# Performance work log

Measured on AMD Instinct MI355X. Metric: run time of the kernel, lower is better.

The kernel has to match this reference:

```python
import jax, jax.numpy as jnp
import numpy as np

KS = 7
HEADS = 8


def _conv1x1(a, w, b):
    # a: (B,Cin,H,W), w: (Cout,Cin), b: (Cout,)
    return jnp.einsum('bchw,oc->bohw', a, w) + b[None, :, None, None]


def _unfold2d(a, ks):
    # a: (B,C,Hp,Wp) -> (B,C,H,W,ks,ks) sliding windows, stride 1
    H = a.shape[2] - ks + 1
    W = a.shape[3] - ks + 1
    ii = jnp.arange(H)[:, None] + jnp.arange(ks)[None, :]  # (H,ks)
    jj = jnp.arange(W)[:, None] + jnp.arange(ks)[None, :]  # (W,ks)
    return a[:, :, ii[:, None, :, None], jj[None, :, None, :]]


def setup_inputs() -> dict:
    key = jax.random.key(0)
    ks = jax.random.split(key, 10)
    B, C, H, W = 4, 128, 56, 56
    x = jax.random.normal(ks[0], (B, C, H, W), dtype=jnp.float32)
    sc = 1.0 / np.sqrt(C)
    q_w = jax.random.normal(ks[1], (C, C), dtype=jnp.float32) * sc
    q_b = jax.random.normal(ks[2], (C,), dtype=jnp.float32) * 0.01
    k_w = jax.random.normal(ks[3], (C, C), dtype=jnp.float32) * sc
    k_b = jax.random.normal(ks[4], (C,), dtype=jnp.float32) * 0.01
    v_w = jax.random.normal(ks[5], (C, C), dtype=jnp.float32) * sc
    v_b = jax.random.normal(ks[6], (C,), dtype=jnp.float32) * 0.01
    rel_h = jax.random.normal(ks[7], (C // 2, KS, 1), dtype=jnp.float32)
    rel_w = jax.random.normal(ks[8], (C // 2, 1, KS), dtype=jnp.float32)
    return {'x': x, 'q_w': q_w, 'q_b': q_b, 'k_w': k_w, 'k_b': k_b,
            'v_w': v_w, 'v_b': v_b, 'rel_h': rel_h, 'rel_w': rel_w}


def reference(x, q_w, q_b, k_w, k_b, v_w, v_b, rel_h, rel_w):
    B, C, H, W = x.shape
    dkh = C // HEADS
    K2 = KS * KS
    pl = (KS - 1) // 2
    pr = KS - 1 - pl
    xp = jnp.pad(x, ((0, 0), (0, 0), (pl, pr), (pl, pr)))

    k = _conv1x1(xp, k_w, k_b)
    v = _conv1x1(xp, v_w, v_b)
    q = _conv1x1(x, q_w, q_b)

    # unfold K/V into (B,C,H,W,KS,KS) then reshape exactly as torch does
    # (this reshape intermixes channel/window axes; replicated faithfully)
    k6 = _unfold2d(k, KS).reshape(B, HEADS, H, W, dkh, K2)
    v6 = _unfold2d(v, KS).reshape(B, HEADS, H, W, dkh, K2)
    q6 = q.reshape(B, HEADS, H, W, dkh, 1)

    # q^T k over the dkh axis -> (B,heads,H,W,KS,KS)
    qk = jnp.einsum('bhxyd,bhxydk->bhxyk', q6[..., 0], k6)
    qk = qk.reshape(B, HEADS, H, W, KS, KS)

    # einsum 'bhxydz,cij->bhxyij' has no shared index: factorizes as
    # (sum over d,z of q) * (sum over c of rel)
    qsum = q6.sum(axis=(4, 5))  # (B,heads,H,W)
    qk = qk + qsum[..., None, None] * rel_h.sum(axis=0)  # (KS,1) broadcast
    qk = qk + qsum[..., None, None] * rel_w.sum(axis=0)  # (1,KS) broadcast

    w = jax.nn.softmax(qk.reshape(B, HEADS, H, W, K2), axis=-1)
    out = jnp.einsum('bhxyk,bhxydk->bhxyd', w, v6)  # (B,heads,H,W,dvh)
    return out.reshape(B, C, H, W)
```

## Files before the change

### kernel.cpp

```cpp
#include <hip/hip_runtime.h>
#include <hip/hip_bf16.h>
#include <math.h>

#define NB    4
#define NC    128
#define NPIX  3136
#define CHW   401408
#define KVP   3968
#define SKS   68
#define STS   19

template <int CTRL, int RM>
__device__ __forceinline__ float dpp_mov(float x, float old) {
    return __int_as_float(__builtin_amdgcn_update_dpp(
        __float_as_int(old), __float_as_int(x), CTRL, RM, 0xf, false));
}
__device__ __forceinline__ float wave_max(float x) {
    x = fmaxf(x, dpp_mov<0x111, 0xf>(x, x));
    x = fmaxf(x, dpp_mov<0x112, 0xf>(x, x));
    x = fmaxf(x, dpp_mov<0x114, 0xf>(x, x));
    x = fmaxf(x, dpp_mov<0x118, 0xf>(x, x));
    x = fmaxf(x, dpp_mov<0x142, 0xa>(x, x));
    x = fmaxf(x, dpp_mov<0x143, 0xc>(x, x));
    return __int_as_float(__builtin_amdgcn_readlane(__float_as_int(x), 63));
}
__device__ __forceinline__ float wave_sum(float x) {
    x = x + dpp_mov<0x111, 0xf>(x, 0.f);
    x = x + dpp_mov<0x112, 0xf>(x, 0.f);
    x = x + dpp_mov<0x114, 0xf>(x, 0.f);
    x = x + dpp_mov<0x118, 0xf>(x, 0.f);
    x = x + dpp_mov<0x142, 0xa>(x, 0.f);
    x = x + dpp_mov<0x143, 0xc>(x, 0.f);
    return __int_as_float(__builtin_amdgcn_readlane(__float_as_int(x), 63));
}

__global__ __launch_bounds__(256) void prep_kernel(
    const float* __restrict__ qw, const float* __restrict__ kw,
    const float* __restrict__ vw,
    const float* __restrict__ kb, const float* __restrict__ vb,
    const float* __restrict__ rel_h, const float* __restrict__ rel_w,
    float* __restrict__ kpad, float* __restrict__ vpad,
    float* __restrict__ w4q, float* __restrict__ w4k, float* __restrict__ w4v,
    float* __restrict__ rb)
{
    int idx = blockIdx.x * 256 + threadIdx.x;
    {
        int img = idx / 708;
        int hl = idx - img * 708;
        int p;
        if (hl < 186) {
            int r = hl / 62;
            p = r * 64 + (hl - r * 62);
        } else if (hl < 372) {
            int j = hl - 186;
            int r = j / 62;
            p = (59 + r) * 64 + (j - r * 62);
        } else {
            int j = hl - 372;
            int r = j / 6, cc = j - r * 6;
            p = (r + 3) * 64 + (cc < 3 ? cc : cc + 56);
        }
        int ch = img & 127;
        size_t o = (size_t)img * KVP + p;
        kpad[o] = kb[ch];
        vpad[o] = vb[ch];
    }
    if (idx < 3 * 16384) {
        int m = idx >> 14;
        int r = idx & 16383;
        int cc = r & 3;
        int t = r >> 2;
        int o = t & 127;
        int c4 = t >> 7;
        const float* src = (m == 0) ? qw : (m == 1) ? kw : vw;
        float* dst = (m == 0) ? w4q : (m == 1) ? w4k : w4v;
        dst[r] = src[o * 128 + c4 * 4 + cc];
    }
    if (idx < 14) {
        const float* src = (idx < 7) ? rel_h : rel_w;
        int off = (idx < 7) ? idx : idx - 7;
        float s = 0.f;
        for (int c = 0; c < 64; ++c) s += src[c * 7 + off];
        rb[idx] = s;
    }
}

__global__ __launch_bounds__(256) void conv_kernel(
    const float* __restrict__ x,
    const float* __restrict__ w4q, const float* __restrict__ w4k,
    const float* __restrict__ w4v,
    const float* __restrict__ qb, const float* __restrict__ kb,
    const float* __restrict__ vb,
    float* __restrict__ q, float* __restrict__ kpad, float* __restrict__ vpad)
{
    __shared__ float sx[128 * 16];
    __shared__ float st[3 * 128 * STS];
    int bid = blockIdx.x;
    int tile = bid % 196;
    int b = bid / 196;
    int pix0 = tile * 16;
    const float* xb = x + b * CHW + pix0;

    for (int i = threadIdx.x; i < 512; i += 256) {
        int c = i >> 2, p4 = (i & 3) * 4;
        *(float4*)(sx + c * 16 + p4) = *(const float4*)(xb + c * NPIX + p4);
    }
    __syncthreads();

    int lane = threadIdx.x & 63;
    int wave = threadIdx.x >> 6;
    int o = wave * 32 + (lane & 31);
    int ph = (lane >> 5) * 8;
    const float4* Wq = (const float4*)w4q + o;
    const float4* Wk = (const float4*)w4k + o;
    const float4* Wv = (const float4*)w4v + o;

    float4 wqc = Wq[0], wkc = Wk[0], wvc = Wv[0];
    float aq[8] = {}, ak[8] = {}, av[8] = {};
    #pragma unroll 1
    for (int c4 = 0; c4 < 32; ++c4) {
        float4 xs[8];
        #pragma unroll
        for (int cc = 0; cc < 4; ++cc) {
            xs[2 * cc]     = *(const float4*)(sx + (c4 * 4 + cc) * 16 + ph);
            xs[2 * cc + 1] = *(const float4*)(sx + (c4 * 4 + cc) * 16 + ph + 4);
        }
        float4 wq4 = wqc, wk4 = wkc, wv4 = wvc;
        if (c4 < 31) {
            wqc = Wq[(c4 + 1) * 128];
            wkc = Wk[(c4 + 1) * 128];
            wvc = Wv[(c4 + 1) * 128];
        }
        float wqr[4] = {wq4.x, wq4.y, wq4.z, wq4.w};
        float wkr[4] = {wk4.x, wk4.y, wk4.z, wk4.w};
        float wvr[4] = {wv4.x, wv4.y, wv4.z, wv4.w};
        #pragma unroll
        for (int cc = 0; cc < 4; ++cc) {
            float4 xa = xs[2 * cc], xc = xs[2 * cc + 1];
            float xv[8] = {xa.x, xa.y, xa.z, xa.w, xc.x, xc.y, xc.z, xc.w};
            #pragma unroll
            for (int p = 0; p < 8; ++p) {
                aq[p] += wqr[cc] * xv[p];
                ak[p] += wkr[cc] * xv[p];
                av[p] += wvr[cc] * xv[p];
            }
        }
    }
    float bq = qb[o], bk = kb[o], bv = vb[o];
    float* wrq = st + o * STS + ph;
    float* wrk = st + 128 * STS + o * STS + ph;
    float* wrv = st + 2 * 128 * STS + o * STS + ph;
    #pragma unroll
    for (int p = 0; p < 8; ++p) {
        wrq[p] = aq[p] + bq;
        wrk[p] = ak[p] + bk;
        wrv[p] = av[p] + bv;
    }
    __syncthreads();

    int pix = threadIdx.x & 15;
    int o8 = (threadIdx.x >> 4) * 8;
    int pp = pix0 + pix;
    int yy = pp / 56, xx = pp - yy * 56;
    int po = (yy + 3) * 64 + xx + 3;
    float* qd = q + b * CHW + pix0 + pix;
    float* kd = kpad + (size_t)b * 128 * KVP + po;
    float* vd = vpad + (size_t)b * 128 * KVP + po;
    #pragma unroll
    for (int i = 0; i < 8; ++i) {
        int r = o8 + i;
        qd[r * NPIX] = st[r * STS + pix];
        kd[(size_t)r * KVP] = st[128 * STS + r * STS + pix];
        vd[(size_t)r * KVP] = st[2 * 128 * STS + r * STS + pix];
    }
}

__global__ __launch_bounds__(256) void attn_kernel(
    const float* __restrict__ q, const float* __restrict__ kpad,
    const float* __restrict__ vpad,
    const float* __restrict__ rb, float* __restrict__ out)
{
    __shared__ __align__(16) float sK[20 * SKS];
    __shared__ __align__(16) float sV[21 * SKS];
    __shared__ float sW[4 * 64];
    int bid = blockIdx.x;
    int qpart = bid & 3;
    int bc = bid >> 2;
    const float* qc = q + bc * NPIX + 784 * qpart;
    float* oc = out + bc * NPIX + 784 * qpart;
    int qr0 = 14 * qpart;
    const float* kp0 = kpad + (size_t)bc * KVP + qr0 * 64;
    const float* vp0 = vpad + (size_t)bc * KVP + qr0 * 64;

    for (int i = threadIdx.x; i < 320; i += 256) {
        int yy = i >> 4, c16 = i & 15;
        if (c16 < 15) {
            float4 kv4 = *(const float4*)(kp0 + yy * 64 + c16 * 4);
            float4 vv4 = *(const float4*)(vp0 + yy * 64 + c16 * 4);
            *(float4*)(sK + yy * SKS + c16 * 4) = kv4;
            *(float4*)(sV + yy * SKS + c16 * 4) = vv4;
        } else {
            float2 kv2 = *(const float2*)(kp0 + yy * 64 + 60);
            float2 vv2 = *(const float2*)(vp0 + yy * 64 + 60);
            *(float2*)(sK + yy * SKS + 60) = kv2;
            *(float2*)(sV + yy * SKS + 60) = vv2;
        }
    }
    for (int i = threadIdx.x; i < SKS; i += 256) sV[20 * SKS + i] = 0.f;

    int lane = threadIdx.x & 63;
    int wave = threadIdx.x >> 6;
    int k2 = min(lane, 48);
    int di = k2 / 7, dj = k2 - di * 7;
    float rbias = rb[di] + rb[7 + dj];
    int koff = di * SKS + dj;
    int t16 = lane & 15, p = lane >> 4;
    float* sWw = sW + wave * 64;

    int ul0 = wave * 16;
    int y0 = 0, x0 = ul0;
    float4 p0 = *(const float4*)(qc + ul0);
    float4 p1 = *(const float4*)(qc + ul0 + 4);
    float4 p2 = *(const float4*)(qc + ul0 + 8);
    float4 p3 = *(const float4*)(qc + ul0 + 12);
    __syncthreads();

    for (int gl = wave; gl < 49; gl += 4) {
        float4 q0 = p0, q1 = p1, q2 = p2, q3 = p3;
        if (gl + 4 < 49) {
            int un = ul0 + 64;
            p0 = *(const float4*)(qc + un);
            p1 = *(const float4*)(qc + un + 4);
            p2 = *(const float4*)(qc + un + 8);
            p3 = *(const float4*)(qc + un + 12);
        }
        float qa[16] = {q0.x, q0.y, q0.z, q0.w, q1.x, q1.y, q1.z, q1.w,
                        q2.x, q2.y, q2.z, q2.w, q3.x, q3.y, q3.z, q3.w};
        float qs = 0.f;
        #pragma unroll
        for (int t = 0; t < 16; ++t) qs += qa[t];

        float acc = 0.f;
        const float* kb_ = sK + y0 * SKS + x0 + koff;
        if (x0 != 48) {
            #pragma unroll
            for (int t = 0; t < 16; ++t) acc += qa[t] * kb_[t];
        } else {
            const float* kb2 = sK + (y0 + 1) * SKS + koff;
            #pragma unroll
            for (int t = 0; t < 8; ++t) acc += qa[t] * kb_[t];
            #pragma unroll
            for (int t = 0; t < 8; ++t) acc += qa[8 + t] * kb2[t];
        }
        float val = (lane < 49) ? (acc + qs * rbias) : -1e30f;

        float mS = wave_max(val);
        float e = __expf(val - mS);
        float sS = wave_sum(e);
        float wgt = e * __builtin_amdgcn_rcpf(sS);
        sWw[lane] = wgt;

        int u = ul0 + t16;
        int yt = u / 56;
        int xt = u - yt * 56;
        const float* vbase = sV + yt * SKS + xt + p * (2 * SKS);
        const float* wbase = sWw + p * 14;
        float o0 = 0.f, o1 = 0.f;
        #pragma unroll
        for (int j = 0; j < 7; ++j) o0 += wbase[j] * vbase[j];
        #pragma unroll
        for (int j = 0; j < 7; ++j) o1 += wbase[7 + j] * vbase[SKS + j];
        float oacc = o0 + o1;
        oacc += __shfl_xor(oacc, 16);
        oacc += __shfl_xor(oacc, 32);
        if (lane < 16) oc[ul0 + lane] = oacc;

        ul0 += 64;
        x0 += 8; y0 += 1;
        if (x0 >= 56) { x0 -= 56; ++y0; }
    }
}

extern "C" void kernel_launch(void* const* d_in, const int* in_sizes, int n_in,
                              void* d_out, int out_size, void* d_ws, size_t ws_size,
                              hipStream_t stream) {
    const float* x     = (const float*)d_in[0];
    const float* qw    = (const float*)d_in[1];
    const float* qb    = (const float*)d_in[2];
    const float* kw    = (const float*)d_in[3];
    const float* kb    = (const float*)d_in[4];
    const float* vw    = (const float*)d_in[5];
    const float* vb    = (const float*)d_in[6];
    const float* rel_h = (const float*)d_in[7];
    const float* rel_w = (const float*)d_in[8];
    float* out = (float*)d_out;

    float* ws   = (float*)d_ws;
    float* kpad = ws;
    float* vpad = kpad + 2031616;
    float* qbuf = vpad + 2031616;
    float* w4q  = qbuf + 1605632;
    float* w4k  = w4q + 16384;
    float* w4v  = w4k + 16384;
    float* rb   = w4v + 16384;

    prep_kernel<<<1416, 256, 0, stream>>>(qw, kw, vw, kb, vb, rel_h, rel_w,
                                          kpad, vpad, w4q, w4k, w4v, rb);
    conv_kernel<<<784, 256, 0, stream>>>(x, w4q, w4k, w4v, qb, kb, vb,
                                         qbuf, kpad, vpad);
    attn_kernel<<<2048, 256, 0, stream>>>(qbuf, kpad, vpad, rb, out);
}
```

Before: 76.37 us.

## Read K/V windows directly from global and drop softmax max reduction

The attention kernel no longer stages the padded K and V rows into LDS behind a block barrier. Each lane now reads its window straight from global memory through the caches. The per-pixel wave-wide max reduction is replaced by a cheap shift built from the bias extremes and the sign of the q-sum, which removes one DPP reduction chain per step. The dot product is also split into two accumulators with a unified boundary-row offset. The trade-off is that softmax stability now depends on the q·k logits staying within exp range, and the scattered global loads rely on cache hits instead of LDS.

```diff
diff --git a/kernel.cpp b/kernel.cpp
--- a/kernel.cpp
+++ b/kernel.cpp
@@ -7,22 +7,12 @@
 #define NPIX  3136
 #define CHW   401408
 #define KVP   3968
-#define SKS   68
 #define STS   19
 
 template <int CTRL, int RM>
 __device__ __forceinline__ float dpp_mov(float x, float old) {
     return __int_as_float(__builtin_amdgcn_update_dpp(
         __float_as_int(old), __float_as_int(x), CTRL, RM, 0xf, false));
-}
-__device__ __forceinline__ float wave_max(float x) {
-    x = fmaxf(x, dpp_mov<0x111, 0xf>(x, x));
-    x = fmaxf(x, dpp_mov<0x112, 0xf>(x, x));
-    x = fmaxf(x, dpp_mov<0x114, 0xf>(x, x));
-    x = fmaxf(x, dpp_mov<0x118, 0xf>(x, x));
-    x = fmaxf(x, dpp_mov<0x142, 0xa>(x, x));
-    x = fmaxf(x, dpp_mov<0x143, 0xc>(x, x));
-    return __int_as_float(__builtin_amdgcn_readlane(__float_as_int(x), 63));
 }
 __device__ __forceinline__ float wave_sum(float x) {
     x = x + dpp_mov<0x111, 0xf>(x, 0.f);
@@ -180,42 +170,33 @@
     const float* __restrict__ vpad,
     const float* __restrict__ rb, float* __restrict__ out)
 {
-    __shared__ __align__(16) float sK[20 * SKS];
-    __shared__ __align__(16) float sV[21 * SKS];
     __shared__ float sW[4 * 64];
     int bid = blockIdx.x;
     int qpart = bid & 3;
     int bc = bid >> 2;
+    int qr0 = 14 * qpart;
     const float* qc = q + bc * NPIX + 784 * qpart;
+    const float* kq = kpad + (size_t)bc * KVP + qr0 * 64;
+    const float* vq = vpad + (size_t)bc * KVP + qr0 * 64;
     float* oc = out + bc * NPIX + 784 * qpart;
-    int qr0 = 14 * qpart;
-    const float* kp0 = kpad + (size_t)bc * KVP + qr0 * 64;
-    const float* vp0 = vpad + (size_t)bc * KVP + qr0 * 64;
-
-    for (int i = threadIdx.x; i < 320; i += 256) {
-        int yy = i >> 4, c16 = i & 15;
-        if (c16 < 15) {
-            float4 kv4 = *(const float4*)(kp0 + yy * 64 + c16 * 4);
-            float4 vv4 = *(const float4*)(vp0 + yy * 64 + c16 * 4);
-            *(float4*)(sK + yy * SKS + c16 * 4) = kv4;
-            *(float4*)(sV + yy * SKS + c16 * 4) = vv4;
-        } else {
-            float2 kv2 = *(const float2*)(kp0 + yy * 64 + 60);
-            float2 vv2 = *(const float2*)(vp0 + yy * 64 + 60);
-            *(float2*)(sK + yy * SKS + 60) = kv2;
-            *(float2*)(sV + yy * SKS + 60) = vv2;
-        }
-    }
-    for (int i = threadIdx.x; i < SKS; i += 256) sV[20 * SKS + i] = 0.f;
 
     int lane = threadIdx.x & 63;
     int wave = threadIdx.x >> 6;
     int k2 = min(lane, 48);
     int di = k2 / 7, dj = k2 - di * 7;
     float rbias = rb[di] + rb[7 + dj];
-    int koff = di * SKS + dj;
+    const float* kwin = kq + di * 64 + dj;
     int t16 = lane & 15, p = lane >> 4;
     float* sWw = sW + wave * 64;
+
+    float rhM = rb[0], rhm = rb[0];
+    #pragma unroll
+    for (int i = 1; i < 7; ++i) { rhM = fmaxf(rhM, rb[i]); rhm = fminf(rhm, rb[i]); }
+    float rwM = rb[7], rwm = rb[7];
+    #pragma unroll
+    for (int i = 8; i < 14; ++i) { rwM = fmaxf(rwM, rb[i]); rwm = fminf(rwm, rb[i]); }
+    float rdMax = rbias - (rhM + rwM);
+    float rdMin = rbias - (rhm + rwm);
 
     int ul0 = wave * 16;
     int y0 = 0, x0 = ul0;
@@ -223,10 +204,24 @@
     float4 p1 = *(const float4*)(qc + ul0 + 4);
     float4 p2 = *(const float4*)(qc + ul0 + 8);
     float4 p3 = *(const float4*)(qc + ul0 + 12);
-    __syncthreads();
 
     for (int gl = wave; gl < 49; gl += 4) {
-        float4 q0 = p0, q1 = p1, q2 = p2, q3 = p3;
+        float qs = (((p0.x + p0.y) + (p0.z + p0.w)) + ((p1.x + p1.y) + (p1.z + p1.w)))
+                 + (((p2.x + p2.y) + (p2.z + p2.w)) + ((p3.x + p3.y) + (p3.z + p3.w)));
+        const float* kp = kwin + y0 * 64 + x0;
+        int d2 = (x0 == 48) ? 16 : 8;
+        const float* kp2 = kp + d2;
+        float a0, a1;
+        a0  = p0.x * kp[0];   a1  = p0.y * kp[1];
+        a0 += p0.z * kp[2];   a1 += p0.w * kp[3];
+        a0 += p1.x * kp[4];   a1 += p1.y * kp[5];
+        a0 += p1.z * kp[6];   a1 += p1.w * kp[7];
+        a0 += p2.x * kp2[0];  a1 += p2.y * kp2[1];
+        a0 += p2.z * kp2[2];  a1 += p2.w * kp2[3];
+        a0 += p3.x * kp2[4];  a1 += p3.y * kp2[5];
+        a0 += p3.z * kp2[6];  a1 += p3.w * kp2[7];
+        float acc = a0 + a1;
+
         if (gl + 4 < 49) {
             int un = ul0 + 64;
             p0 = *(const float4*)(qc + un);
@@ -234,28 +229,10 @@
             p2 = *(const float4*)(qc + un + 8);
             p3 = *(const float4*)(qc + un + 12);
         }
-        float qa[16] = {q0.x, q0.y, q0.z, q0.w, q1.x, q1.y, q1.z, q1.w,
-                        q2.x, q2.y, q2.z, q2.w, q3.x, q3.y, q3.z, q3.w};
-        float qs = 0.f;
-        #pragma unroll
-        for (int t = 0; t < 16; ++t) qs += qa[t];
-
-        float acc = 0.f;
-        const float* kb_ = sK + y0 * SKS + x0 + koff;
-        if (x0 != 48) {
-            #pragma unroll
-            for (int t = 0; t < 16; ++t) acc += qa[t] * kb_[t];
-        } else {
-            const float* kb2 = sK + (y0 + 1) * SKS + koff;
-            #pragma unroll
-            for (int t = 0; t < 8; ++t) acc += qa[t] * kb_[t];
-            #pragma unroll
-            for (int t = 0; t < 8; ++t) acc += qa[8 + t] * kb2[t];
-        }
-        float val = (lane < 49) ? (acc + qs * rbias) : -1e30f;
-
-        float mS = wave_max(val);
-        float e = __expf(val - mS);
+
+        float rd = (qs > 0.f) ? rdMax : rdMin;
+        float ex = fmaf(qs, rd, acc);
+        float e = (lane < 49) ? __expf(ex) : 0.f;
         float sS = wave_sum(e);
         float wgt = e * __builtin_amdgcn_rcpf(sS);
         sWw[lane] = wgt;
@@ -263,13 +240,13 @@
         int u = ul0 + t16;
         int yt = u / 56;
         int xt = u - yt * 56;
-        const float* vbase = sV + yt * SKS + xt + p * (2 * SKS);
+        const float* vb0 = vq + (yt + 2 * p) * 64 + xt;
         const float* wbase = sWw + p * 14;
         float o0 = 0.f, o1 = 0.f;
         #pragma unroll
-        for (int j = 0; j < 7; ++j) o0 += wbase[j] * vbase[j];
-        #pragma unroll
-        for (int j = 0; j < 7; ++j) o1 += wbase[7 + j] * vbase[SKS + j];
+        for (int j = 0; j < 7; ++j) o0 += wbase[j] * vb0[j];
+        #pragma unroll
+        for (int j = 0; j < 7; ++j) o1 += wbase[7 + j] * vb0[64 + j];
         float oacc = o0 + o1;
         oacc += __shfl_xor(oacc, 16);
         oacc += __shfl_xor(oacc, 32);
```

After: 76.37 us. About the same (-0.0%).
